# Performance work log

Hardware: AMD Instinct MI355X
Metric: run time of the kernel (lower is better)

## Reference

```python
import jax, jax.numpy as jnp
import numpy as np

GROUP = 16   # self.group
K = 3        # self.k (top-3 motif rows)


def _unfold3(x):
    # nn.Unfold(kernel_size=3): [B,C,H,W] -> [B, C*9, (H-2)*(W-2)]
    # torch channel ordering: c-major, then kernel offsets row-major.
    B, C, H, W = x.shape
    Ho, Wo = H - 2, W - 2
    pats = jnp.stack([x[:, :, i:i + Ho, j:j + Wo]
                      for i in range(3) for j in range(3)], axis=2)  # [B,C,9,Ho,Wo]
    return pats.reshape(B, C * 9, Ho * Wo)


def _fold3(y, H, W):
    # nn.Fold(output_size=(H,W), kernel_size=3): sum overlapping patches back.
    B, C9, L = y.shape
    C = C9 // 9
    Ho, Wo = H - 2, W - 2
    y = y.reshape(B, C, 3, 3, Ho, Wo)
    out = jnp.zeros((B, C, H, W), y.dtype)
    for i in range(3):
        for j in range(3):
            out = out.at[:, :, i:i + Ho, j:j + Wo].add(y[:, :, i, j])
    return out


def _group_motif(xg, H, W):
    motif = _unfold3(xg)                                  # [B,P,L], P = Cg*9
    B, P, L = motif.shape
    # torch.cdist (p=2) between the P rows, via the Gram trick.
    sq = jnp.sum(motif * motif, axis=-1)                  # [B,P]
    gram = jnp.einsum('bpl,bql->bpq', motif, motif)       # [B,P,P]
    d2 = sq[:, :, None] + sq[:, None, :] - 2.0 * gram
    dist = jnp.sqrt(jnp.maximum(d2, 0.0))
    eye = jnp.eye(P, dtype=bool)[None]
    dist = jnp.where(eye, jnp.inf, dist)                  # diagonal := inf
    # topk(k=1, largest=False) == argmin over last dim
    min_idx = jnp.argmin(dist, axis=-1)                   # [B,P] int
    # torch.unique(return_counts=True) over the whole tensor (flattened over batch)
    counts = jnp.bincount(min_idx.ravel(), length=P)      # [P] int
    # sort counts descending, take first K uniques -> lax.top_k
    top_c, top_i = jax.lax.top_k(counts, K)               # [K],[K]
    total = jnp.sum(top_c).astype(motif.dtype)
    rows = motif[:, top_i, :]                             # [B,K,L] gathered motif rows
    cf = top_c.astype(motif.dtype)
    motif_new = jnp.zeros_like(motif)
    for o in range(K):
        # torch: motif * motif[:, u_o].unsqueeze(1) * c_o // total  (floor division)
        motif_new = motif_new + jnp.floor(motif * rows[:, o][:, None, :] * cf[o] / total)
    return _fold3(motif_new, H, W)


def setup_inputs() -> dict:
    key = jax.random.key(0)
    feature = jax.random.normal(key, (2, 256, 192, 192), dtype=jnp.float32)
    return {"feature": feature}


def reference(feature):
    B, C, H, W = feature.shape
    chunks = jnp.split(feature, GROUP, axis=1)
    outs = [_group_motif(g, H, W) for g in chunks]
    return jnp.concatenate(outs, axis=1)                  # [B, C, H, W]
```

## Files before the change

### kernel.cpp

```cpp
#include <hip/hip_runtime.h>
#include <math.h>

#define NB 2
#define NC 256
#define CG 16
#define HH 192
#define WW 192
#define HO 190
#define PP 144

typedef float v2f __attribute__((ext_vector_type(2)));

#define SMEM_FLOATS 7348

__global__ __launch_bounds__(192, 2) void gram_kernel(const float* __restrict__ x,
                                                      double* __restrict__ gram)
{
    __shared__ float smem[SMEM_FLOATS];
    float* const red_s = smem + 2548;

    const int v = threadIdx.x;

    const int bid = blockIdx.x;
    const int vx = bid & 7;
    const int tq = bid >> 3;
    const int idxw = tq / 36;
    const int rr0 = tq - idxw * 36;
    const int hg = idxw * 8 + vx;
    const int bg = hg >> 1;
    int r = rr0 + 36 * (hg & 1);
    int c2 = 0;
    while (r >= (c2 + 2) / 2) { r -= (c2 + 2) / 2; ++c2; }
    const int c1a = 2 * r;
    int c1b = 2 * r + 1;
    const bool bval = (c1b <= c2);
    if (!bval) c1b = c2;
    const int b = bg >> 4, g = bg & 15;

    const float* __restrict__ xa  = x + ((size_t)(b * NC + g * CG + c1a)) * (HH * WW);
    const float* __restrict__ xb  = x + ((size_t)(b * NC + g * CG + c1b)) * (HH * WW);
    const float* __restrict__ x2g = x + ((size_t)(b * NC + g * CG + c2 )) * (HH * WW);

    if (v < 148) smem[(v >> 2) * 196 + (v & 3)] = 0.f;

    v2f mid2[25];
#pragma unroll
    for (int o = 0; o < 25; ++o) mid2[o] = (v2f){0.f, 0.f};

    float win[6][5];
    v2f cab[6];
#pragma unroll
    for (int k = 0; k < 6; ++k)
        cab[k] = (v2f){xa[(size_t)(2 + k) * WW + v], xb[(size_t)(2 + k) * WW + v]};

    const float* pa = xa + (size_t)8 * WW + v;
    const float* pb = xb + (size_t)8 * WW + v;
    int lds_off;

#define USTEP6(P, WPF, GPF)                                                   \
    {                                                                         \
        const v2f ab = cab[(P)];                                              \
        if (GPF) cab[(P)] = (v2f){pa[(P) * WW], pb[(P) * WW]};                \
        if (WPF) {                                                            \
            const float* wr = &smem[lds_off];                                 \
            _Pragma("unroll")                                                 \
            for (int dj = 0; dj < 5; ++dj)                                    \
                win[((P) + 5) % 6][dj] = wr[dj];                              \
        }                                                                     \
        lds_off += 196;                                                       \
        _Pragma("unroll")                                                     \
        for (int kk = 0; kk < 5; ++kk) {                                      \
            _Pragma("unroll")                                                 \
            for (int dj = 0; dj < 5; ++dj) {                                  \
                const float xv = win[((P) + kk) % 6][dj];                     \
                mid2[kk * 5 + dj] = __builtin_elementwise_fma(                \
                    ab, (v2f){xv, xv}, mid2[kk * 5 + dj]);                    \
            }                                                                 \
        }                                                                     \
    }

    for (int band = 0; band < 7; ++band) {
        const bool full = (band < 6);
        const int u0 = 2 + band * 30;
        const int row0 = u0 - 2;
        const int limit = (full ? 35 : 12) * 48;
        __syncthreads();
        for (int it = 0; it < (full ? 9 : 3); ++it) {
            const int idx = it * 192 + v;
            if (idx < limit) {
                const int rr2 = idx / 48;
                const int c4 = (idx - rr2 * 48) * 4;
                const float4 val = *(const float4*)(x2g + (size_t)(row0 + rr2) * WW + c4);
                *(float4*)(&smem[rr2 * 196 + 4 + c4]) = val;
            }
        }
        __syncthreads();
        if (band == 0) {
#pragma unroll
            for (int k = 0; k < 5; ++k)
#pragma unroll
            for (int dj = 0; dj < 5; ++dj)
                win[k][dj] = smem[k * 196 + 2 + v + dj];
        }
        lds_off = 5 * 196 + 2 + v;

        if (full) {
            for (int it = 0; it < 5; ++it) {
                USTEP6(0, 1, 1) USTEP6(1, 1, 1) USTEP6(2, 1, 1)
                USTEP6(3, 1, 1) USTEP6(4, 1, 1) USTEP6(5, 1, 1)
                pa += 6 * WW; pb += 6 * WW;
            }
        } else {
            USTEP6(0, 1, 1) USTEP6(1, 1, 1) USTEP6(2, 1, 0)
            USTEP6(3, 1, 0) USTEP6(4, 1, 0) USTEP6(5, 1, 0)
            USTEP6(0, 1, 0) USTEP6(1, 0, 0)
        }
    }
#undef USTEP6

    __syncthreads();
    for (int i = 0; i < 12; ++i) {
        const int ar = (i < 6) ? (i - 2) : (188 + i - 6);
        const float val = (ar >= 0 && ar <= 191) ? x2g[(size_t)ar * WW + v] : 0.f;
        smem[i * 196 + 4 + v] = val;
    }
    __syncthreads();

    double* const gp = gram + (size_t)bg * (PP * PP);

#pragma unroll
    for (int i1 = 0; i1 < 3; ++i1) {
        const int ra = (i1 == 0) ? 0 : ((i1 == 1) ? 1 : 190);
        const int rb = (i1 == 0) ? 1 : ((i1 == 1) ? 190 : 191);
#pragma unroll
        for (int c = 0; c < 2; ++c) {
            const float* __restrict__ xc = (c == 0) ? xa : xb;
            const float xra = xc[(size_t)ra * WW + v];
            const float xrb = xc[(size_t)rb * WW + v];
#pragma unroll
            for (int k = 0; k < 5; ++k) {
                const int bufa = (ra < 2) ? (ra + k) : (ra + k - 184);
                const int bufb = (rb < 2) ? (rb + k) : (rb + k - 184);
#pragma unroll
                for (int dj = 0; dj < 5; ++dj) {
                    const int q = k * 5 + dj;
                    float cw = (c == 0) ? mid2[q].x : mid2[q].y;
                    cw = fmaf(xra, smem[bufa * 196 + 2 + v + dj], cw);
                    cw = fmaf(xrb, smem[bufb * 196 + 2 + v + dj], cw);
                    red_s[v * 25 + q] = cw;
                }
            }
            __syncthreads();
            float e0 = 0.f, e1 = 0.f, e190 = 0.f, e191 = 0.f;
            if (v < 25) {
                e0   = red_s[0 * 25 + v];
                e1   = red_s[1 * 25 + v];
                e190 = red_s[190 * 25 + v];
                e191 = red_s[191 * 25 + v];
            }
            __syncthreads();
#pragma unroll
            for (int s = 96; s >= 3; s >>= 1) {
                for (int idx = v; idx < s * 25; idx += 192) {
                    const int vv = idx / 25, o = idx - vv * 25;
                    red_s[vv * 25 + o] += red_s[(vv + s) * 25 + o];
                }
                __syncthreads();
            }
            if (v < 25 && (c == 0 || bval)) {
                const int di = v / 5 - 2, dj = v - (v / 5) * 5 - 2;
                const int i2 = i1 + di;
                if (i2 >= 0 && i2 <= 2) {
                    const float S = red_s[0 * 25 + v] + red_s[1 * 25 + v] + red_s[2 * 25 + v];
                    const int c1 = (c == 0) ? c1a : c1b;
#pragma unroll
                    for (int j1 = 0; j1 < 3; ++j1) {
                        const int j2 = j1 + dj;
                        if (j2 < 0 || j2 > 2) continue;
                        const float W = S - ((j1 == 0) ? (e190 + e191)
                                          : (j1 == 1) ? (e0 + e191)
                                                      : (e0 + e1));
                        const int p = c1 * 9 + i1 * 3 + j1;
                        const int q = c2 * 9 + i2 * 3 + j2;
                        gp[p * PP + q] = (double)W;
                        if (c1 != c2) gp[q * PP + p] = (double)W;
                    }
                }
            }
            __syncthreads();
        }
    }
}

__global__ __launch_bounds__(320) void topk_kernel(const double* __restrict__ gram,
                                                   float* __restrict__ pf,
                                                   int* __restrict__ pi)
{
    const int g = blockIdx.x;
    __shared__ double sdiag[2][PP];
    __shared__ int counts[PP];
    const int tid = threadIdx.x;
    if (tid < PP) counts[tid] = 0;
    if (tid < 2 * PP) {
        const int b = tid / PP, p = tid % PP;
        const double* gb = gram + (size_t)(b * 16 + g) * (PP * PP);
        sdiag[b][p] = gb[p * PP + p];
    }
    __syncthreads();
    if (tid < 2 * PP) {
        const int b = tid / PP, p = tid % PP;
        const double* row = gram + ((size_t)(b * 16 + g) * PP + p) * PP;
        const double sp = sdiag[b][p];
        double best = 1e300;
        int bi = 0;
        for (int q = 0; q < PP; ++q) {
            if (q == p) continue;
            const double d2 = sp + sdiag[b][q] - 2.0 * row[q];
            if (d2 < best) { best = d2; bi = q; }
        }
        atomicAdd(&counts[bi], 1);
    }
    __syncthreads();
    if (tid == 0) {
        int sel[3], cv[3];
        for (int o = 0; o < 3; ++o) {
            int bc = -1, bp = 0;
            for (int p = 0; p < PP; ++p) {
                bool taken = false;
                for (int u = 0; u < o; ++u) if (sel[u] == p) taken = true;
                if (!taken && counts[p] > bc) { bc = counts[p]; bp = p; }
            }
            sel[o] = bp; cv[o] = bc;
        }
        const int tot = cv[0] + cv[1] + cv[2];
        for (int o = 0; o < 3; ++o) {
            pf[g * 4 + o] = (float)cv[o];
            pi[g * 4 + o] = sel[o];
        }
        pf[g * 4 + 3] = (float)tot;
    }
}

template <bool EDGE>
__device__ __forceinline__ void motif_quad(const float* __restrict__ x,
                                           const float* __restrict__ pf,
                                           const int* __restrict__ pi,
                                           float* __restrict__ out,
                                           int b, int ch, int h, int w0)
{
    const int g = ch >> 4;
    const size_t base = ((size_t)(b * NC + ch)) * (HH * WW);
    const float4 xv4 = *(const float4*)(x + base + (size_t)h * WW + w0);
    const float xs[4] = {xv4.x, xv4.y, xv4.z, xv4.w};
    float acc[4] = {0.f, 0.f, 0.f, 0.f};
    const float total = pf[g * 4 + 3];
    const double invd = 1.0 / (double)total;

#pragma unroll
    for (int o = 0; o < 3; ++o) {
        const int p = pi[g * 4 + o];
        const float cff = pf[g * 4 + o];
        const int co = p / 9;
        const int kk = p - co * 9;
        const int io = kk / 3, jo = kk - (kk / 3) * 3;
        const float* Rb = x + ((size_t)(b * NC + g * CG + co)) * (HH * WW);
#pragma unroll
        for (int i = 0; i < 3; ++i) {
            const int ho = h - i;
            bool rowok = true;
            int hr = ho + io;
            if (EDGE) {
                rowok = (ho >= 0) && (ho < HO);
                hr = hr < 0 ? 0 : (hr > HH - 1 ? HH - 1 : hr);
            }
            const float* row = Rb + (size_t)hr * WW;
            float rv[6];
#pragma unroll
            for (int u = 0; u < 6; ++u) {
                int col = w0 - 2 + jo + u;
                if (EDGE) col = col < 0 ? 0 : (col > WW - 1 ? WW - 1 : col);
                rv[u] = row[col];
            }
#pragma unroll
            for (int j = 0; j < 3; ++j)
#pragma unroll
            for (int q = 0; q < 4; ++q) {
                const float r2 = rv[q - j + 2];
                const float t1 = xs[q] * r2;
                const float t2 = t1 * cff;
                const float qf = (float)((double)t2 * invd);
                const float vfl = floorf(qf);
                if (EDGE) {
                    const int wo = w0 + q - j;
                    const bool ok = rowok && (wo >= 0) && (wo < HO);
                    acc[q] += ok ? vfl : 0.f;
                } else {
                    acc[q] += vfl;
                }
            }
        }
    }
    float4 ov = make_float4(acc[0], acc[1], acc[2], acc[3]);
    *(float4*)(out + base + (size_t)h * WW + w0) = ov;
}

__global__ __launch_bounds__(256) void out_interior(const float* __restrict__ x,
                                                    const float* __restrict__ pf,
                                                    const int* __restrict__ pi,
                                                    float* __restrict__ out)
{
    const int gid = blockIdx.x * 256 + threadIdx.x;
    const int w4i = gid % 46;
    int t = gid / 46;
    const int h = 2 + t % 188; t /= 188;
    const int ch = t & 255;
    const int b = t >> 8;
    motif_quad<false>(x, pf, pi, out, b, ch, h, (w4i + 1) * 4);
}

__global__ __launch_bounds__(256) void out_edge(const float* __restrict__ x,
                                                const float* __restrict__ pf,
                                                const int* __restrict__ pi,
                                                float* __restrict__ out)
{
    const int gid = blockIdx.x * 256 + threadIdx.x;
    const int e = gid % 568;
    int t = gid / 568;
    const int ch = t & 255;
    const int b = t >> 8;
    int h, w4;
    if (e < 192) {
        const int hs = e / 48;
        h = (hs < 2) ? hs : 188 + hs;
        w4 = e % 48;
    } else {
        const int e2 = e - 192;
        h = 2 + (e2 >> 1);
        w4 = (e2 & 1) ? 47 : 0;
    }
    motif_quad<true>(x, pf, pi, out, b, ch, h, w4 * 4);
}

extern "C" void kernel_launch(void* const* d_in, const int* in_sizes, int n_in,
                              void* d_out, int out_size, void* d_ws, size_t ws_size,
                              hipStream_t stream)
{
    const float* x = (const float*)d_in[0];
    float* out = (float*)d_out;

    double* gram = (double*)d_ws;
    const size_t gram_bytes = (size_t)32 * PP * PP * sizeof(double);
    float* pf = (float*)((char*)d_ws + gram_bytes);
    int* pi = (int*)((char*)d_ws + gram_bytes + 256);

    gram_kernel<<<2304, 192, 0, stream>>>(x, gram);
    topk_kernel<<<16, 320, 0, stream>>>(gram, pf, pi);
    out_interior<<<17296, 256, 0, stream>>>(x, pf, pi, out);
    out_edge<<<1136, 256, 0, stream>>>(x, pf, pi, out);
}
```

Measured before the change: 405.3 us.

## Split gram kernel column offsets across two thread halves to raise occupancy

Doubles the gram kernel block to 384 threads. The two halves of each block split the five horizontal offsets, three for the first half and two for the second, so each thread keeps 15 instead of 25 v2f accumulators and a smaller window. The cooperative band loads, the edge-row staging and the reduction loops are re-strided for the larger block. This lowers register pressure to allow more resident waves. In exchange, every thread redundantly loads the same column values for both halves, and the halves carry unequal work.

```diff
diff --git a/kernel.cpp b/kernel.cpp
--- a/kernel.cpp
+++ b/kernel.cpp
@@ -13,13 +13,16 @@
 
 #define SMEM_FLOATS 7348
 
-__global__ __launch_bounds__(192, 2) void gram_kernel(const float* __restrict__ x,
+__global__ __launch_bounds__(384, 3) void gram_kernel(const float* __restrict__ x,
                                                       double* __restrict__ gram)
 {
     __shared__ float smem[SMEM_FLOATS];
     float* const red_s = smem + 2548;
 
     const int v = threadIdx.x;
+    const int half = (v >= 192) ? 1 : 0;
+    const int v2 = v - half * 192;
+    const int wbase = 2 + v2 + half * 3;
 
     const int bid = blockIdx.x;
     const int vx = bid & 7;
@@ -43,39 +46,60 @@
 
     if (v < 148) smem[(v >> 2) * 196 + (v & 3)] = 0.f;
 
-    v2f mid2[25];
-#pragma unroll
-    for (int o = 0; o < 25; ++o) mid2[o] = (v2f){0.f, 0.f};
-
-    float win[6][5];
+    v2f mid2[15];
+#pragma unroll
+    for (int o = 0; o < 15; ++o) mid2[o] = (v2f){0.f, 0.f};
+
+    float win[6][3];
     v2f cab[6];
 #pragma unroll
     for (int k = 0; k < 6; ++k)
-        cab[k] = (v2f){xa[(size_t)(2 + k) * WW + v], xb[(size_t)(2 + k) * WW + v]};
-
-    const float* pa = xa + (size_t)8 * WW + v;
-    const float* pb = xb + (size_t)8 * WW + v;
+        cab[k] = (v2f){xa[(size_t)(2 + k) * WW + v2], xb[(size_t)(2 + k) * WW + v2]};
+
+    const float* pa = xa + (size_t)8 * WW + v2;
+    const float* pb = xb + (size_t)8 * WW + v2;
     int lds_off;
 
-#define USTEP6(P, WPF, GPF)                                                   \
+#define USTEP6(P, WPF, GPF, ND)                                               \
     {                                                                         \
         const v2f ab = cab[(P)];                                              \
         if (GPF) cab[(P)] = (v2f){pa[(P) * WW], pb[(P) * WW]};                \
         if (WPF) {                                                            \
-            const float* wr = &smem[lds_off];                                 \
             _Pragma("unroll")                                                 \
-            for (int dj = 0; dj < 5; ++dj)                                    \
-                win[((P) + 5) % 6][dj] = wr[dj];                              \
+            for (int d = 0; d < (ND); ++d)                                    \
+                win[((P) + 5) % 6][d] = smem[lds_off + d];                    \
         }                                                                     \
         lds_off += 196;                                                       \
         _Pragma("unroll")                                                     \
         for (int kk = 0; kk < 5; ++kk) {                                      \
             _Pragma("unroll")                                                 \
-            for (int dj = 0; dj < 5; ++dj) {                                  \
-                const float xv = win[((P) + kk) % 6][dj];                     \
-                mid2[kk * 5 + dj] = __builtin_elementwise_fma(                \
-                    ab, (v2f){xv, xv}, mid2[kk * 5 + dj]);                    \
+            for (int d = 0; d < (ND); ++d) {                                  \
+                const float xv = win[((P) + kk) % 6][d];                      \
+                mid2[kk * (ND) + d] = __builtin_elementwise_fma(              \
+                    ab, (v2f){xv, xv}, mid2[kk * (ND) + d]);                  \
             }                                                                 \
+        }                                                                     \
+    }
+
+#define BANDBODY(ND)                                                          \
+    {                                                                         \
+        if (band == 0) {                                                      \
+            _Pragma("unroll")                                                 \
+            for (int k = 0; k < 5; ++k)                                       \
+                _Pragma("unroll")                                             \
+                for (int d = 0; d < (ND); ++d)                                \
+                    win[k][d] = smem[k * 196 + wbase + d];                    \
+        }                                                                     \
+        if (full) {                                                           \
+            for (int it = 0; it < 5; ++it) {                                  \
+                USTEP6(0,1,1,ND) USTEP6(1,1,1,ND) USTEP6(2,1,1,ND)            \
+                USTEP6(3,1,1,ND) USTEP6(4,1,1,ND) USTEP6(5,1,1,ND)            \
+                pa += 6 * WW; pb += 6 * WW;                                   \
+            }                                                                 \
+        } else {                                                              \
+            USTEP6(0,1,1,ND) USTEP6(1,1,1,ND) USTEP6(2,1,0,ND)                \
+            USTEP6(3,1,0,ND) USTEP6(4,1,0,ND) USTEP6(5,1,0,ND)                \
+            USTEP6(0,1,0,ND) USTEP6(1,0,0,ND)                                 \
         }                                                                     \
     }
 
@@ -85,8 +109,8 @@
         const int row0 = u0 - 2;
         const int limit = (full ? 35 : 12) * 48;
         __syncthreads();
-        for (int it = 0; it < (full ? 9 : 3); ++it) {
-            const int idx = it * 192 + v;
+        for (int it = 0; it < (full ? 5 : 2); ++it) {
+            const int idx = it * 384 + v;
             if (idx < limit) {
                 const int rr2 = idx / 48;
                 const int c4 = (idx - rr2 * 48) * 4;
@@ -95,38 +119,39 @@
             }
         }
         __syncthreads();
-        if (band == 0) {
-#pragma unroll
-            for (int k = 0; k < 5; ++k)
-#pragma unroll
-            for (int dj = 0; dj < 5; ++dj)
-                win[k][dj] = smem[k * 196 + 2 + v + dj];
-        }
-        lds_off = 5 * 196 + 2 + v;
-
-        if (full) {
-            for (int it = 0; it < 5; ++it) {
-                USTEP6(0, 1, 1) USTEP6(1, 1, 1) USTEP6(2, 1, 1)
-                USTEP6(3, 1, 1) USTEP6(4, 1, 1) USTEP6(5, 1, 1)
-                pa += 6 * WW; pb += 6 * WW;
-            }
-        } else {
-            USTEP6(0, 1, 1) USTEP6(1, 1, 1) USTEP6(2, 1, 0)
-            USTEP6(3, 1, 0) USTEP6(4, 1, 0) USTEP6(5, 1, 0)
-            USTEP6(0, 1, 0) USTEP6(1, 0, 0)
-        }
+        lds_off = 5 * 196 + wbase;
+
+        if (!half) BANDBODY(3) else BANDBODY(2)
     }
 #undef USTEP6
+#undef BANDBODY
 
     __syncthreads();
-    for (int i = 0; i < 12; ++i) {
+#pragma unroll
+    for (int ii = 0; ii < 6; ++ii) {
+        const int i = half * 6 + ii;
         const int ar = (i < 6) ? (i - 2) : (188 + i - 6);
-        const float val = (ar >= 0 && ar <= 191) ? x2g[(size_t)ar * WW + v] : 0.f;
-        smem[i * 196 + 4 + v] = val;
+        const float val = (ar >= 0 && ar <= 191) ? x2g[(size_t)ar * WW + v2] : 0.f;
+        smem[i * 196 + 4 + v2] = val;
     }
     __syncthreads();
 
     double* const gp = gram + (size_t)bg * (PP * PP);
+
+#define EPIWRITE(ND, DJ0)                                                     \
+    _Pragma("unroll")                                                         \
+    for (int k = 0; k < 5; ++k) {                                             \
+        const int bufa = (ra < 2) ? (ra + k) : (ra + k - 184);                \
+        const int bufb = (rb < 2) ? (rb + k) : (rb + k - 184);                \
+        _Pragma("unroll")                                                     \
+        for (int d = 0; d < (ND); ++d) {                                      \
+            const v2f m = mid2[k * (ND) + d];                                 \
+            float cw = (c == 0) ? m.x : m.y;                                  \
+            cw = fmaf(xra, smem[bufa * 196 + wbase + d], cw);                 \
+            cw = fmaf(xrb, smem[bufb * 196 + wbase + d], cw);                 \
+            red_s[v2 * 25 + k * 5 + (DJ0) + d] = cw;                          \
+        }                                                                     \
+    }
 
 #pragma unroll
     for (int i1 = 0; i1 < 3; ++i1) {
@@ -135,21 +160,9 @@
 #pragma unroll
         for (int c = 0; c < 2; ++c) {
             const float* __restrict__ xc = (c == 0) ? xa : xb;
-            const float xra = xc[(size_t)ra * WW + v];
-            const float xrb = xc[(size_t)rb * WW + v];
-#pragma unroll
-            for (int k = 0; k < 5; ++k) {
-                const int bufa = (ra < 2) ? (ra + k) : (ra + k - 184);
-                const int bufb = (rb < 2) ? (rb + k) : (rb + k - 184);
-#pragma unroll
-                for (int dj = 0; dj < 5; ++dj) {
-                    const int q = k * 5 + dj;
-                    float cw = (c == 0) ? mid2[q].x : mid2[q].y;
-                    cw = fmaf(xra, smem[bufa * 196 + 2 + v + dj], cw);
-                    cw = fmaf(xrb, smem[bufb * 196 + 2 + v + dj], cw);
-                    red_s[v * 25 + q] = cw;
-                }
-            }
+            const float xra = xc[(size_t)ra * WW + v2];
+            const float xrb = xc[(size_t)rb * WW + v2];
+            if (!half) EPIWRITE(3, 0) else EPIWRITE(2, 3)
             __syncthreads();
             float e0 = 0.f, e1 = 0.f, e190 = 0.f, e191 = 0.f;
             if (v < 25) {
@@ -161,7 +174,7 @@
             __syncthreads();
 #pragma unroll
             for (int s = 96; s >= 3; s >>= 1) {
-                for (int idx = v; idx < s * 25; idx += 192) {
+                for (int idx = v; idx < s * 25; idx += 384) {
                     const int vv = idx / 25, o = idx - vv * 25;
                     red_s[vv * 25 + o] += red_s[(vv + s) * 25 + o];
                 }
@@ -190,6 +203,7 @@
             __syncthreads();
         }
     }
+#undef EPIWRITE
 }
 
 __global__ __launch_bounds__(320) void topk_kernel(const double* __restrict__ gram,
@@ -353,7 +367,7 @@
     float* pf = (float*)((char*)d_ws + gram_bytes);
     int* pi = (int*)((char*)d_ws + gram_bytes + 256);
 
-    gram_kernel<<<2304, 192, 0, stream>>>(x, gram);
+    gram_kernel<<<2304, 384, 0, stream>>>(x, gram);
     topk_kernel<<<16, 320, 0, stream>>>(gram, pf, pi);
     out_interior<<<17296, 256, 0, stream>>>(x, pf, pi, out);
     out_edge<<<1136, 256, 0, stream>>>(x, pf, pi, out);
```

Measured after the change: 486.5 us. 20.0% more time.

## Split gram kernel rows into two halves with atomic double accumulation

Applied to the files above, without the earlier changes.

The gram kernel's row sweep is split into two halves, so twice as many blocks each handle about 94 rows. Partial Gram entries are combined with double-precision atomicAdd into a buffer that is zeroed by a memset first. Only the first half handles the boundary-row corrections. This adds parallelism and shortens each block's serial loop, at the cost of an extra memset, atomics, and a duplicated reduction epilogue per block.

```diff
diff --git a/kernel.cpp b/kernel.cpp
--- a/kernel.cpp
+++ b/kernel.cpp
@@ -22,8 +22,12 @@
     const int v = threadIdx.x;
 
     const int bid = blockIdx.x;
-    const int vx = bid & 7;
-    const int tq = bid >> 3;
+    const int sblk = (bid >= 2304) ? 1 : 0;
+    const int rb = bid - sblk * 2304;
+    const int ustart = 2 + sblk * 94;
+
+    const int vx = rb & 7;
+    const int tq = rb >> 3;
     const int idxw = tq / 36;
     const int rr0 = tq - idxw * 36;
     const int hg = idxw * 8 + vx;
@@ -51,10 +55,11 @@
     v2f cab[6];
 #pragma unroll
     for (int k = 0; k < 6; ++k)
-        cab[k] = (v2f){xa[(size_t)(2 + k) * WW + v], xb[(size_t)(2 + k) * WW + v]};
-
-    const float* pa = xa + (size_t)8 * WW + v;
-    const float* pb = xb + (size_t)8 * WW + v;
+        cab[k] = (v2f){xa[(size_t)(ustart + k) * WW + v],
+                       xb[(size_t)(ustart + k) * WW + v]};
+
+    const float* pa = xa + (size_t)(ustart + 6) * WW + v;
+    const float* pb = xb + (size_t)(ustart + 6) * WW + v;
     int lds_off;
 
 #define USTEP6(P, WPF, GPF)                                                   \
@@ -79,13 +84,13 @@
         }                                                                     \
     }
 
-    for (int band = 0; band < 7; ++band) {
-        const bool full = (band < 6);
-        const int u0 = 2 + band * 30;
+    for (int band = 0; band < 4; ++band) {
+        const bool full = (band < 3);
+        const int u0 = ustart + band * 30;
         const int row0 = u0 - 2;
-        const int limit = (full ? 35 : 12) * 48;
+        const int limit = (full ? 35 : 8) * 48;
         __syncthreads();
-        for (int it = 0; it < (full ? 9 : 3); ++it) {
+        for (int it = 0; it < (full ? 9 : 2); ++it) {
             const int idx = it * 192 + v;
             if (idx < limit) {
                 const int rr2 = idx / 48;
@@ -111,18 +116,18 @@
                 pa += 6 * WW; pb += 6 * WW;
             }
         } else {
-            USTEP6(0, 1, 1) USTEP6(1, 1, 1) USTEP6(2, 1, 0)
-            USTEP6(3, 1, 0) USTEP6(4, 1, 0) USTEP6(5, 1, 0)
-            USTEP6(0, 1, 0) USTEP6(1, 0, 0)
+            USTEP6(0, 1, 0) USTEP6(1, 1, 0) USTEP6(2, 1, 0) USTEP6(3, 0, 0)
         }
     }
 #undef USTEP6
 
     __syncthreads();
-    for (int i = 0; i < 12; ++i) {
-        const int ar = (i < 6) ? (i - 2) : (188 + i - 6);
-        const float val = (ar >= 0 && ar <= 191) ? x2g[(size_t)ar * WW + v] : 0.f;
-        smem[i * 196 + 4 + v] = val;
+    if (sblk == 0) {
+        for (int i = 0; i < 12; ++i) {
+            const int ar = (i < 6) ? (i - 2) : (188 + i - 6);
+            const float val = (ar >= 0 && ar <= 191) ? x2g[(size_t)ar * WW + v] : 0.f;
+            smem[i * 196 + 4 + v] = val;
+        }
     }
     __syncthreads();
 
@@ -131,23 +136,33 @@
 #pragma unroll
     for (int i1 = 0; i1 < 3; ++i1) {
         const int ra = (i1 == 0) ? 0 : ((i1 == 1) ? 1 : 190);
-        const int rb = (i1 == 0) ? 1 : ((i1 == 1) ? 190 : 191);
+        const int rb2 = (i1 == 0) ? 1 : ((i1 == 1) ? 190 : 191);
 #pragma unroll
         for (int c = 0; c < 2; ++c) {
             const float* __restrict__ xc = (c == 0) ? xa : xb;
-            const float xra = xc[(size_t)ra * WW + v];
-            const float xrb = xc[(size_t)rb * WW + v];
-#pragma unroll
-            for (int k = 0; k < 5; ++k) {
-                const int bufa = (ra < 2) ? (ra + k) : (ra + k - 184);
-                const int bufb = (rb < 2) ? (rb + k) : (rb + k - 184);
+            if (sblk == 0) {
+                const float xra = xc[(size_t)ra * WW + v];
+                const float xrb = xc[(size_t)rb2 * WW + v];
+#pragma unroll
+                for (int k = 0; k < 5; ++k) {
+                    const int bufa = (ra < 2) ? (ra + k) : (ra + k - 184);
+                    const int bufb = (rb2 < 2) ? (rb2 + k) : (rb2 + k - 184);
+#pragma unroll
+                    for (int dj = 0; dj < 5; ++dj) {
+                        const int q = k * 5 + dj;
+                        float cw = (c == 0) ? mid2[q].x : mid2[q].y;
+                        cw = fmaf(xra, smem[bufa * 196 + 2 + v + dj], cw);
+                        cw = fmaf(xrb, smem[bufb * 196 + 2 + v + dj], cw);
+                        red_s[v * 25 + q] = cw;
+                    }
+                }
+            } else {
+#pragma unroll
+                for (int k = 0; k < 5; ++k)
 #pragma unroll
                 for (int dj = 0; dj < 5; ++dj) {
                     const int q = k * 5 + dj;
-                    float cw = (c == 0) ? mid2[q].x : mid2[q].y;
-                    cw = fmaf(xra, smem[bufa * 196 + 2 + v + dj], cw);
-                    cw = fmaf(xrb, smem[bufb * 196 + 2 + v + dj], cw);
-                    red_s[v * 25 + q] = cw;
+                    red_s[v * 25 + q] = (c == 0) ? mid2[q].x : mid2[q].y;
                 }
             }
             __syncthreads();
@@ -182,8 +197,8 @@
                                                       : (e0 + e1));
                         const int p = c1 * 9 + i1 * 3 + j1;
                         const int q = c2 * 9 + i2 * 3 + j2;
-                        gp[p * PP + q] = (double)W;
-                        if (c1 != c2) gp[q * PP + p] = (double)W;
+                        atomicAdd(&gp[p * PP + q], (double)W);
+                        if (c1 != c2) atomicAdd(&gp[q * PP + p], (double)W);
                     }
                 }
             }
@@ -353,7 +368,9 @@
     float* pf = (float*)((char*)d_ws + gram_bytes);
     int* pi = (int*)((char*)d_ws + gram_bytes + 256);
 
-    gram_kernel<<<2304, 192, 0, stream>>>(x, gram);
+    hipMemsetAsync(gram, 0, gram_bytes, stream);
+
+    gram_kernel<<<4608, 192, 0, stream>>>(x, gram);
     topk_kernel<<<16, 320, 0, stream>>>(gram, pf, pi);
     out_interior<<<17296, 256, 0, stream>>>(x, pf, pi, out);
     out_edge<<<1136, 256, 0, stream>>>(x, pf, pi, out);
```

After: 472.2 us. 1.17x slower.
